# Optimization experiments

Hardware: AMD Instinct MI355X
Metric: run time of the kernel (lower is better)

Reference implementation:

```python
import jax, jax.numpy as jnp
import numpy as np

B, N, M, C, H, NNZ = 64, 2048, 2048, 64, 128, 32768


def setup_inputs() -> dict:
    key = jax.random.key(0)
    ks = jax.random.split(key, 7)
    x = jax.random.normal(ks[0], (B * N, H), dtype=jnp.float32)
    batch = jnp.repeat(jnp.arange(B, dtype=jnp.int32), N)  # sorted graph ids
    d_rows = jax.random.randint(ks[1], (B, NNZ), 0, M, dtype=jnp.int32)
    d_cols = jax.random.randint(ks[2], (B, NNZ), 0, N, dtype=jnp.int32)
    d_vals = jax.random.normal(ks[3], (B, NNZ), dtype=jnp.float32) * (1.0 / np.sqrt(16.0))
    d_index = jax.random.randint(ks[4], (B, M), 0, C, dtype=jnp.int32)
    w_scale = 1.0 / np.sqrt(3 * H)
    Wq = jax.random.normal(ks[5], (3 * H, H), dtype=jnp.float32) * w_scale
    Wk = jax.random.normal(ks[6], (3 * H, H), dtype=jnp.float32) * w_scale
    Wv = jax.random.normal(jax.random.fold_in(key, 7), (3 * H, H), dtype=jnp.float32) * w_scale
    return {"x": x, "batch": batch, "batch_size": B, "d_rows": d_rows,
            "d_cols": d_cols, "d_vals": d_vals, "d_index": d_index,
            "Wq": Wq, "Wk": Wk, "Wv": Wv}


def _per_graph(xg, rows, cols, vals, idx, Wq, Wk, Wv):
    # spmm: coefs[r] = sum_e vals[e] * xg[cols[e]] for rows[e] == r  -> [M, H]
    coefs = jax.ops.segment_sum(vals[:, None] * xg[cols], rows, num_segments=M)
    # three segment poolings over cluster index -> each [C, H]
    s = jax.ops.segment_sum(coefs, idx, num_segments=C)
    cnt = jax.ops.segment_sum(jnp.ones((M,), coefs.dtype), idx, num_segments=C)
    mean = s / jnp.maximum(cnt, 1.0)[:, None]
    mx = jax.ops.segment_max(coefs, idx, num_segments=C)
    x_dec = jnp.concatenate([mean, mx, s], axis=1)  # [C, 3H]
    # small self-attention over clusters (linear layers without bias)
    Q = x_dec @ Wq
    K = x_dec @ Wk
    V = x_dec @ Wv
    dist = jax.nn.softmax((Q @ K.T) * (1.0 / np.sqrt(H)), axis=-1)
    return (dist @ V).reshape(-1)  # [C*H]


def reference(x, batch, batch_size, d_rows, d_cols, d_vals, d_index, Wq, Wk, Wv):
    # nodes are sorted by graph with equal graph size N, so x[batch==i] == xb[i]
    xb = x.reshape(batch_size, N, H)
    out = jax.vmap(_per_graph, in_axes=(0, 0, 0, 0, 0, None, None, None))(
        xb, d_rows, d_cols, d_vals, d_index, Wq, Wk, Wv)
    return out  # [B, C*H] == torch.vstack of per-graph flattened attentions
```

## Files before the change

### kernel.cpp

```cpp
#include <hip/hip_runtime.h>
#include <hip/hip_fp16.h>

#define BG 64
#define NN 2048
#define MM 2048
#define CC 64
#define HH 128
#define NNZE 32768
#define TH 384

__global__ __launch_bounds__(256) void cvt_x_kernel(const float* __restrict__ x,
                                                    uint* __restrict__ xh) {
    int tid = blockIdx.x * 256 + threadIdx.x;
    const float4* x4 = (const float4*)x;
    float4 a = x4[2 * tid], b = x4[2 * tid + 1];
    __half2 h0 = __float22half2_rn(make_float2(a.x, a.y));
    __half2 h1 = __float22half2_rn(make_float2(a.z, a.w));
    __half2 h2 = __float22half2_rn(make_float2(b.x, b.y));
    __half2 h3 = __float22half2_rn(make_float2(b.z, b.w));
    uint4 o;
    o.x = *(uint*)&h0;
    o.y = *(uint*)&h1;
    o.z = *(uint*)&h2;
    o.w = *(uint*)&h3;
    ((uint4*)xh)[tid] = o;
}

__global__ __launch_bounds__(1024) void prep_graph_kernel(const int* __restrict__ d_rows,
                                                          const int* __restrict__ d_cols,
                                                          const float* __restrict__ d_vals,
                                                          const int* __restrict__ d_index,
                                                          int* __restrict__ cnt_clu_g,
                                                          int* __restrict__ off_clu_g,
                                                          int* __restrict__ row_edge_off_g,
                                                          int2* __restrict__ epack) {
    __shared__ int cnt_clu_s[CC], off_clu_s[CC], fill_clu_s[CC];
    __shared__ int rlist_s[MM];
    __shared__ int cnt_row_s[MM];
    __shared__ int off_row_s[MM];
    __shared__ int fill_row_s[MM];
    __shared__ int wsum[16];
    int g = blockIdx.x, t = threadIdx.x;
    int lane = t & 63, w = t >> 6;

    cnt_row_s[t] = 0; cnt_row_s[t + 1024] = 0;
    fill_row_s[t] = 0; fill_row_s[t + 1024] = 0;
    if (t < CC) { cnt_clu_s[t] = 0; fill_clu_s[t] = 0; }
    int idx0 = d_index[(g << 11) + t];
    int idx1 = d_index[(g << 11) + t + 1024];
    __syncthreads();

    const int* rows_g = d_rows + ((size_t)g << 15);
#pragma unroll
    for (int it = 0; it < 32; it++) atomicAdd(&cnt_row_s[rows_g[it * 1024 + t]], 1);
    atomicAdd(&cnt_clu_s[idx0], 1);
    atomicAdd(&cnt_clu_s[idx1], 1);
    __syncthreads();

    if (t < CC) {
        int v = cnt_clu_s[t], incl = v;
#pragma unroll
        for (int d = 1; d < 64; d <<= 1) {
            int u = __shfl_up(incl, d);
            if (t >= d) incl += u;
        }
        off_clu_s[t] = incl - v;
        cnt_clu_g[(g << 6) + t] = v;
        off_clu_g[(g << 6) + t] = incl - v;
    }
    __syncthreads();

    {
        int s0 = atomicAdd(&fill_clu_s[idx0], 1);
        rlist_s[off_clu_s[idx0] + s0] = t;
        int s1 = atomicAdd(&fill_clu_s[idx1], 1);
        rlist_s[off_clu_s[idx1] + s1] = t + 1024;
    }
    __syncthreads();

    int r0 = rlist_s[2 * t], r1 = rlist_s[2 * t + 1];
    int c0 = cnt_row_s[r0], c1 = cnt_row_s[r1];
    int s = c0 + c1;
    int incl = s;
#pragma unroll
    for (int d = 1; d < 64; d <<= 1) {
        int u = __shfl_up(incl, d);
        if (lane >= d) incl += u;
    }
    if (lane == 63) wsum[w] = incl;
    __syncthreads();
    if (t < 16) {
        int v = wsum[t], iv = v;
#pragma unroll
        for (int d = 1; d < 16; d <<= 1) {
            int u = __shfl_up(iv, d);
            if (t >= d) iv += u;
        }
        wsum[t] = iv - v;
    }
    __syncthreads();
    {
        int base = wsum[w] + incl - s;
        int* reo = row_edge_off_g + g * (MM + 1);
        reo[2 * t] = base;
        reo[2 * t + 1] = base + c0;
        off_row_s[r0] = base;
        off_row_s[r1] = base + c0;
        if (t == 0) reo[MM] = NNZE;
    }
    __syncthreads();

    const int* cols_g = d_cols + ((size_t)g << 15);
    const float* vals_g = d_vals + ((size_t)g << 15);
    int2* ep_g = epack + ((size_t)g << 15);
#pragma unroll
    for (int it = 0; it < 32; it++) {
        int e = it * 1024 + t;
        int r = rows_g[e];
        int slot = atomicAdd(&fill_row_s[r], 1);
        int flag = (slot == cnt_row_s[r] - 1) ? (int)0x80000000 : 0;
        ep_g[off_row_s[r] + slot] = make_int2(cols_g[e] | flag, __float_as_int(vals_g[e]));
    }
}

__global__ __launch_bounds__(64) void spmm_pool_kernel(const uint* __restrict__ xh,
                                                       const int* __restrict__ cnt_clu,
                                                       const int* __restrict__ off_clu,
                                                       const int* __restrict__ row_edge_off,
                                                       const int2* __restrict__ epack,
                                                       float* __restrict__ xdec) {
    int bid = blockIdx.x;
    int l = bid >> 3;
    int g = ((bid & 7) << 3) + (l >> 6);
    int c = l & 63;
    int h = threadIdx.x;
    int gc = (g << 6) + c;
    int rcnt = cnt_clu[gc];
    int j0 = off_clu[gc];
    const int* reo = row_edge_off + g * (MM + 1) + j0;
    int ebase = reo[0];
    int etot = reo[rcnt] - ebase;
    const long long* ep = (const long long*)(epack + ((size_t)g << 15)) + ebase;
    const uint* xg = xh + ((size_t)g << 17);
    float2 coef = make_float2(0.f, 0.f), sum = make_float2(0.f, 0.f);
    float2 mx = make_float2(-__builtin_inff(), -__builtin_inff());
    int e = 0;
    for (; e + 16 <= etot; e += 16) {
        long long q[16];
#pragma unroll
        for (int k = 0; k < 16; k++) q[k] = __builtin_nontemporal_load(&ep[e + k]);
        uint xv[16];
#pragma unroll
        for (int k = 0; k < 16; k++)
            xv[k] = xg[(((uint)(int)q[k] & 0x7FFFFFFFu) << 6) + h];
#pragma unroll
        for (int k = 0; k < 16; k++) {
            float v = __int_as_float((int)(q[k] >> 32));
            float2 f = __half22float2(*(__half2*)&xv[k]);
            coef.x = fmaf(v, f.x, coef.x);
            coef.y = fmaf(v, f.y, coef.y);
            if ((int)q[k] < 0) {
                sum.x += coef.x; sum.y += coef.y;
                mx.x = fmaxf(mx.x, coef.x); mx.y = fmaxf(mx.y, coef.y);
                coef.x = 0.f; coef.y = 0.f;
            }
        }
    }
    for (; e < etot; e++) {
        long long q = ep[e];
        uint xv = xg[(((uint)(int)q & 0x7FFFFFFFu) << 6) + h];
        float v = __int_as_float((int)(q >> 32));
        float2 f = __half22float2(*(__half2*)&xv);
        coef.x = fmaf(v, f.x, coef.x);
        coef.y = fmaf(v, f.y, coef.y);
        if ((int)q < 0) {
            sum.x += coef.x; sum.y += coef.y;
            mx.x = fmaxf(mx.x, coef.x); mx.y = fmaxf(mx.y, coef.y);
            coef.x = 0.f; coef.y = 0.f;
        }
    }
    int az = 0;
    for (int j = h; j < rcnt; j += 64) az |= (reo[j + 1] == reo[j]);
    if (__ballot(az) != 0ULL) {
        mx.x = fmaxf(mx.x, 0.f);
        mx.y = fmaxf(mx.y, 0.f);
    }
    float inv = 1.f / (float)(rcnt > 0 ? rcnt : 1);
    float* xd = xdec + (size_t)gc * TH;
    *(float2*)&xd[2 * h] = make_float2(sum.x * inv, sum.y * inv);
    *(float2*)&xd[HH + 2 * h] = mx;
    *(float2*)&xd[2 * HH + 2 * h] = sum;
}

__global__ __launch_bounds__(256) void qkv_kernel(const float* __restrict__ xdec,
                                                  const float* __restrict__ Wq,
                                                  const float* __restrict__ Wk,
                                                  const float* __restrict__ Wv,
                                                  float* __restrict__ QKV) {
    __shared__ float As[16][68];
    __shared__ float Bs[16][64];
    int bx = blockIdx.x, by = blockIdx.y;
    int t = threadIdx.x;
    int tx = t & 15, ty = t >> 4;
    const float* W = (by < 2) ? Wq : (by < 4) ? Wk : Wv;
    int cbase = (by & 1) * 64;
    int r0 = bx * 64;
    float acc[4][4] = {};
    int lrow = t >> 2, lk4 = (t & 3) * 4;
    for (int k0 = 0; k0 < TH; k0 += 16) {
        float4 av = *(const float4*)&xdec[(size_t)(r0 + lrow) * TH + k0 + lk4];
        As[lk4][lrow] = av.x;
        As[lk4 + 1][lrow] = av.y;
        As[lk4 + 2][lrow] = av.z;
        As[lk4 + 3][lrow] = av.w;
        *(float4*)&Bs[ty][tx * 4] = *(const float4*)&W[(size_t)(k0 + ty) * HH + cbase + tx * 4];
        __syncthreads();
#pragma unroll
        for (int k = 0; k < 16; k++) {
            float4 a = *(float4*)&As[k][ty * 4];
            float4 b = *(float4*)&Bs[k][tx * 4];
            float ar[4] = {a.x, a.y, a.z, a.w};
            float br[4] = {b.x, b.y, b.z, b.w};
#pragma unroll
            for (int i = 0; i < 4; i++)
#pragma unroll
                for (int j = 0; j < 4; j++) acc[i][j] = fmaf(ar[i], br[j], acc[i][j]);
        }
        __syncthreads();
    }
#pragma unroll
    for (int i = 0; i < 4; i++) {
        *(float4*)&QKV[(size_t)(r0 + ty * 4 + i) * TH + by * 64 + tx * 4] =
            make_float4(acc[i][0], acc[i][1], acc[i][2], acc[i][3]);
    }
}

__global__ __launch_bounds__(256) void attn_kernel(const float* __restrict__ QKV,
                                                   float* __restrict__ out) {
    __shared__ float Qs[16][132];
    __shared__ float sc[16][68];
    int g = blockIdx.x;
    int q0 = blockIdx.y * 16;
    int t = threadIdx.x;
    const float* base = QKV + (size_t)(g * CC) * TH;
    for (int u = t; u < 512; u += 256) {
        int i = u >> 5, cc = u & 31;
        *(float4*)&Qs[i][cc * 4] = *(const float4*)&base[(size_t)(q0 + i) * TH + cc * 4];
    }
    __syncthreads();
    {
        int j = t & 63, iq = t >> 6;
        float a0 = 0, a1 = 0, a2 = 0, a3 = 0;
        const float* Krow = base + (size_t)j * TH + HH;
#pragma unroll 4
        for (int cc = 0; cc < 32; cc++) {
            float4 kv = *(const float4*)&Krow[cc * 4];
            float4 q0v = *(float4*)&Qs[iq][cc * 4];
            float4 q1v = *(float4*)&Qs[4 + iq][cc * 4];
            float4 q2v = *(float4*)&Qs[8 + iq][cc * 4];
            float4 q3v = *(float4*)&Qs[12 + iq][cc * 4];
            a0 += kv.x * q0v.x + kv.y * q0v.y + kv.z * q0v.z + kv.w * q0v.w;
            a1 += kv.x * q1v.x + kv.y * q1v.y + kv.z * q1v.z + kv.w * q1v.w;
            a2 += kv.x * q2v.x + kv.y * q2v.y + kv.z * q2v.z + kv.w * q2v.w;
            a3 += kv.x * q3v.x + kv.y * q3v.y + kv.z * q3v.z + kv.w * q3v.w;
        }
        const float scale = 0.08838834764831845f;
        sc[iq][j] = a0 * scale;
        sc[4 + iq][j] = a1 * scale;
        sc[8 + iq][j] = a2 * scale;
        sc[12 + iq][j] = a3 * scale;
    }
    __syncthreads();
    {
        int i = t >> 4, l = t & 15;
        float4 sv = *(float4*)&sc[i][l * 4];
        float m = fmaxf(fmaxf(sv.x, sv.y), fmaxf(sv.z, sv.w));
#pragma unroll
        for (int d = 1; d < 16; d <<= 1) m = fmaxf(m, __shfl_xor(m, d));
        float4 p;
        p.x = __expf(sv.x - m);
        p.y = __expf(sv.y - m);
        p.z = __expf(sv.z - m);
        p.w = __expf(sv.w - m);
        float s = p.x + p.y + p.z + p.w;
#pragma unroll
        for (int d = 1; d < 16; d <<= 1) s += __shfl_xor(s, d);
        float inv = 1.0f / s;
        p.x *= inv; p.y *= inv; p.z *= inv; p.w *= inv;
        *(float4*)&sc[i][l * 4] = p;
    }
    __syncthreads();
    {
        int i = t >> 4, hq = t & 15;
        const float* Vbase = base + 2 * HH;
        float acc[8] = {};
        for (int j = 0; j < 64; j++) {
            float d = sc[i][j];
            float4 v0 = *(const float4*)&Vbase[(size_t)j * TH + hq * 8];
            float4 v1 = *(const float4*)&Vbase[(size_t)j * TH + hq * 8 + 4];
            acc[0] = fmaf(d, v0.x, acc[0]);
            acc[1] = fmaf(d, v0.y, acc[1]);
            acc[2] = fmaf(d, v0.z, acc[2]);
            acc[3] = fmaf(d, v0.w, acc[3]);
            acc[4] = fmaf(d, v1.x, acc[4]);
            acc[5] = fmaf(d, v1.y, acc[5]);
            acc[6] = fmaf(d, v1.z, acc[6]);
            acc[7] = fmaf(d, v1.w, acc[7]);
        }
        float* op = out + (size_t)g * (CC * HH) + (size_t)(q0 + i) * HH + hq * 8;
        *(float4*)&op[0] = make_float4(acc[0], acc[1], acc[2], acc[3]);
        *(float4*)&op[4] = make_float4(acc[4], acc[5], acc[6], acc[7]);
    }
}

extern "C" void kernel_launch(void* const* d_in, const int* in_sizes, int n_in,
                              void* d_out, int out_size, void* d_ws, size_t ws_size,
                              hipStream_t stream) {
    const float* x = (const float*)d_in[0];
    const int* d_rows = (const int*)d_in[3];
    const int* d_cols = (const int*)d_in[4];
    const float* d_vals = (const float*)d_in[5];
    const int* d_index = (const int*)d_in[6];
    const float* Wq = (const float*)d_in[7];
    const float* Wk = (const float*)d_in[8];
    const float* Wv = (const float*)d_in[9];
    float* out = (float*)d_out;

    char* ws = (char*)d_ws;
    size_t o = 0;
    uint* xh = (uint*)(ws + o); o += (size_t)BG * NN * (HH / 2) * 4;
    int2* epack = (int2*)(ws + o); o += (size_t)BG * NNZE * 8;
    int* row_edge_off = (int*)(ws + o); o += (size_t)BG * (MM + 1) * 4;
    int* cnt_clu = (int*)(ws + o); o += (size_t)BG * CC * 4;
    int* off_clu = (int*)(ws + o); o += (size_t)BG * CC * 4;
    float* xdec = (float*)(ws + o); o += (size_t)BG * CC * TH * 4;
    float* QKV = (float*)(ws + o); o += (size_t)BG * CC * TH * 4;

    cvt_x_kernel<<<BG * NN * HH / 8 / 256, 256, 0, stream>>>(x, xh);
    prep_graph_kernel<<<BG, 1024, 0, stream>>>(d_rows, d_cols, d_vals, d_index,
                                               cnt_clu, off_clu, row_edge_off, epack);
    spmm_pool_kernel<<<BG * CC, 64, 0, stream>>>(xh, cnt_clu, off_clu, row_edge_off,
                                                 epack, xdec);
    qkv_kernel<<<dim3(64, 6), 256, 0, stream>>>(xdec, Wq, Wk, Wv, QKV);
    attn_kernel<<<dim3(BG, 4), 256, 0, stream>>>(QKV, out);
}
```

Before: 313.2 us.

## Split graph preprocessing into count, scan and bin kernels across sub-blocks

Replaces the single per-graph prep kernel (64 blocks) with three kernels: a per-quarter row/cluster count kernel, a per-graph scan that builds per-sub-block row offsets, and a per-quarter binning kernel that scatters packed edges. This spreads the atomic-heavy edge loops over four times as many blocks so more CUs are used. It costs two extra launches and extra global round-trips for the intermediate count and offset arrays.

```diff
diff --git a/kernel.cpp b/kernel.cpp
--- a/kernel.cpp
+++ b/kernel.cpp
@@ -26,39 +26,61 @@
     ((uint4*)xh)[tid] = o;
 }
 
-__global__ __launch_bounds__(1024) void prep_graph_kernel(const int* __restrict__ d_rows,
-                                                          const int* __restrict__ d_cols,
-                                                          const float* __restrict__ d_vals,
+__global__ __launch_bounds__(1024) void prep_count_kernel(const int* __restrict__ d_rows,
                                                           const int* __restrict__ d_index,
-                                                          int* __restrict__ cnt_clu_g,
-                                                          int* __restrict__ off_clu_g,
-                                                          int* __restrict__ row_edge_off_g,
-                                                          int2* __restrict__ epack) {
+                                                          int* __restrict__ cnt_blk,
+                                                          int* __restrict__ cnt_clu_blk) {
+    __shared__ int cnt_row_s[MM];
+    __shared__ int cnt_clu_s[CC];
+    int gb = blockIdx.x;
+    int g = gb >> 2, b = gb & 3;
+    int t = threadIdx.x;
+    cnt_row_s[t] = 0;
+    cnt_row_s[t + 1024] = 0;
+    if (t < CC) cnt_clu_s[t] = 0;
+    __syncthreads();
+    const int* rows_g = d_rows + ((size_t)g << 15) + (b << 13);
+#pragma unroll
+    for (int it = 0; it < 8; it++) atomicAdd(&cnt_row_s[rows_g[it * 1024 + t]], 1);
+    if (t < 512) atomicAdd(&cnt_clu_s[d_index[(g << 11) + (b << 9) + t]], 1);
+    __syncthreads();
+    int* cb = cnt_blk + (size_t)gb * MM;
+    cb[t] = cnt_row_s[t];
+    cb[t + 1024] = cnt_row_s[t + 1024];
+    if (t < CC) cnt_clu_blk[gb * CC + t] = cnt_clu_s[t];
+}
+
+__global__ __launch_bounds__(1024) void prep_scan_kernel(const int* __restrict__ d_index,
+                                                         const int* __restrict__ cnt_blk,
+                                                         const int* __restrict__ cnt_clu_blk,
+                                                         int* __restrict__ cnt_clu_g,
+                                                         int* __restrict__ off_clu_g,
+                                                         int* __restrict__ row_edge_off_g,
+                                                         int* __restrict__ off_row_blk,
+                                                         int* __restrict__ end_pos) {
     __shared__ int cnt_clu_s[CC], off_clu_s[CC], fill_clu_s[CC];
     __shared__ int rlist_s[MM];
-    __shared__ int cnt_row_s[MM];
+    __shared__ int rowtot_s[MM];
+    __shared__ int blk1_s[MM], blk2_s[MM], blk3_s[MM];
     __shared__ int off_row_s[MM];
-    __shared__ int fill_row_s[MM];
     __shared__ int wsum[16];
     int g = blockIdx.x, t = threadIdx.x;
     int lane = t & 63, w = t >> 6;
 
-    cnt_row_s[t] = 0; cnt_row_s[t + 1024] = 0;
-    fill_row_s[t] = 0; fill_row_s[t + 1024] = 0;
-    if (t < CC) { cnt_clu_s[t] = 0; fill_clu_s[t] = 0; }
-    int idx0 = d_index[(g << 11) + t];
-    int idx1 = d_index[(g << 11) + t + 1024];
-    __syncthreads();
-
-    const int* rows_g = d_rows + ((size_t)g << 15);
-#pragma unroll
-    for (int it = 0; it < 32; it++) atomicAdd(&cnt_row_s[rows_g[it * 1024 + t]], 1);
-    atomicAdd(&cnt_clu_s[idx0], 1);
-    atomicAdd(&cnt_clu_s[idx1], 1);
-    __syncthreads();
-
+    const int* cb = cnt_blk + ((size_t)g << 2) * MM;
+    for (int r = t; r < MM; r += 1024) {
+        int c0 = cb[r], c1 = cb[MM + r], c2 = cb[2 * MM + r], c3 = cb[3 * MM + r];
+        blk1_s[r] = c0;
+        blk2_s[r] = c0 + c1;
+        blk3_s[r] = c0 + c1 + c2;
+        rowtot_s[r] = c0 + c1 + c2 + c3;
+    }
     if (t < CC) {
-        int v = cnt_clu_s[t], incl = v;
+        const int* ccb = cnt_clu_blk + (g << 2) * CC;
+        int v = ccb[t] + ccb[CC + t] + ccb[2 * CC + t] + ccb[3 * CC + t];
+        cnt_clu_s[t] = v;
+        fill_clu_s[t] = 0;
+        int incl = v;
 #pragma unroll
         for (int d = 1; d < 64; d <<= 1) {
             int u = __shfl_up(incl, d);
@@ -68,6 +90,8 @@
         cnt_clu_g[(g << 6) + t] = v;
         off_clu_g[(g << 6) + t] = incl - v;
     }
+    int idx0 = d_index[(g << 11) + t];
+    int idx1 = d_index[(g << 11) + t + 1024];
     __syncthreads();
 
     {
@@ -79,7 +103,7 @@
     __syncthreads();
 
     int r0 = rlist_s[2 * t], r1 = rlist_s[2 * t + 1];
-    int c0 = cnt_row_s[r0], c1 = cnt_row_s[r1];
+    int c0 = rowtot_s[r0], c1 = rowtot_s[r1];
     int s = c0 + c1;
     int incl = s;
 #pragma unroll
@@ -110,16 +134,51 @@
     }
     __syncthreads();
 
-    const int* cols_g = d_cols + ((size_t)g << 15);
-    const float* vals_g = d_vals + ((size_t)g << 15);
-    int2* ep_g = epack + ((size_t)g << 15);
-#pragma unroll
-    for (int it = 0; it < 32; it++) {
+    int* ob = off_row_blk + ((size_t)g << 2) * MM;
+    int* epp = end_pos + (size_t)g * MM;
+    for (int r = t; r < MM; r += 1024) {
+        int orr = off_row_s[r];
+        ob[r] = orr;
+        ob[MM + r] = orr + blk1_s[r];
+        ob[2 * MM + r] = orr + blk2_s[r];
+        ob[3 * MM + r] = orr + blk3_s[r];
+        epp[r] = orr + rowtot_s[r];
+    }
+}
+
+__global__ __launch_bounds__(1024) void prep_bin_kernel(const int* __restrict__ d_rows,
+                                                        const int* __restrict__ d_cols,
+                                                        const float* __restrict__ d_vals,
+                                                        const int* __restrict__ off_row_blk,
+                                                        const int* __restrict__ end_pos,
+                                                        int2* __restrict__ epack) {
+    __shared__ int off_s[MM];
+    __shared__ int end_s[MM];
+    __shared__ int fill_s[MM];
+    int gb = blockIdx.x;
+    int g = gb >> 2, b = gb & 3;
+    int t = threadIdx.x;
+    const int* ob = off_row_blk + (size_t)gb * MM;
+    const int* epp = end_pos + (size_t)g * MM;
+    off_s[t] = ob[t];
+    off_s[t + 1024] = ob[t + 1024];
+    end_s[t] = epp[t];
+    end_s[t + 1024] = epp[t + 1024];
+    fill_s[t] = 0;
+    fill_s[t + 1024] = 0;
+    __syncthreads();
+    const int* rows_g = d_rows + ((size_t)g << 15) + (b << 13);
+    const int* cols_g = d_cols + ((size_t)g << 15) + (b << 13);
+    const float* vals_g = d_vals + ((size_t)g << 15) + (b << 13);
+    int2* epg = epack + ((size_t)g << 15);
+#pragma unroll
+    for (int it = 0; it < 8; it++) {
         int e = it * 1024 + t;
         int r = rows_g[e];
-        int slot = atomicAdd(&fill_row_s[r], 1);
-        int flag = (slot == cnt_row_s[r] - 1) ? (int)0x80000000 : 0;
-        ep_g[off_row_s[r] + slot] = make_int2(cols_g[e] | flag, __float_as_int(vals_g[e]));
+        int slot = atomicAdd(&fill_s[r], 1);
+        int pos = off_s[r] + slot;
+        int flag = (pos == end_s[r] - 1) ? (int)0x80000000 : 0;
+        epg[pos] = make_int2(cols_g[e] | flag, __float_as_int(vals_g[e]));
     }
 }
 
@@ -330,6 +389,10 @@
     size_t o = 0;
     uint* xh = (uint*)(ws + o); o += (size_t)BG * NN * (HH / 2) * 4;
     int2* epack = (int2*)(ws + o); o += (size_t)BG * NNZE * 8;
+    int* cnt_blk = (int*)(ws + o); o += (size_t)BG * 4 * MM * 4;
+    int* off_row_blk = (int*)(ws + o); o += (size_t)BG * 4 * MM * 4;
+    int* end_pos = (int*)(ws + o); o += (size_t)BG * MM * 4;
+    int* cnt_clu_blk = (int*)(ws + o); o += (size_t)BG * 4 * CC * 4;
     int* row_edge_off = (int*)(ws + o); o += (size_t)BG * (MM + 1) * 4;
     int* cnt_clu = (int*)(ws + o); o += (size_t)BG * CC * 4;
     int* off_clu = (int*)(ws + o); o += (size_t)BG * CC * 4;
@@ -337,8 +400,12 @@
     float* QKV = (float*)(ws + o); o += (size_t)BG * CC * TH * 4;
 
     cvt_x_kernel<<<BG * NN * HH / 8 / 256, 256, 0, stream>>>(x, xh);
-    prep_graph_kernel<<<BG, 1024, 0, stream>>>(d_rows, d_cols, d_vals, d_index,
-                                               cnt_clu, off_clu, row_edge_off, epack);
+    prep_count_kernel<<<BG * 4, 1024, 0, stream>>>(d_rows, d_index, cnt_blk, cnt_clu_blk);
+    prep_scan_kernel<<<BG, 1024, 0, stream>>>(d_index, cnt_blk, cnt_clu_blk,
+                                              cnt_clu, off_clu, row_edge_off,
+                                              off_row_blk, end_pos);
+    prep_bin_kernel<<<BG * 4, 1024, 0, stream>>>(d_rows, d_cols, d_vals,
+                                                 off_row_blk, end_pos, epack);
     spmm_pool_kernel<<<BG * CC, 64, 0, stream>>>(xh, cnt_clu, off_clu, row_edge_off,
                                                  epack, xdec);
     qkv_kernel<<<dim3(64, 6), 256, 0, stream>>>(xdec, Wq, Wk, Wv, QKV);
```

After: 277.0 us. 1.13x faster.
